# Optimization experiments

Hardware: AMD Instinct MI355X
Metric: run time of the kernel (lower is better)

The kernel has to match this reference:

```python
import jax, jax.numpy as jnp
import numpy as np

INT8_MAX = 127.0

def _quant_ste(x, axis):
    """Dynamic symmetric int8 fake-quant along `axis` (per-channel scales).
    Returns dequantized values; math matches int8 dot * scales (AQT-style)."""
    amax = jnp.max(jnp.abs(x), axis=axis, keepdims=True)
    scale = jnp.maximum(amax, 1e-6) / INT8_MAX
    q = jnp.clip(jnp.round(x / scale), -INT8_MAX, INT8_MAX)
    return q * scale

def setup_inputs() -> dict:
    key = jax.random.key(0)
    k1, k2 = jax.random.split(key)
    inputs = jax.random.normal(k1, (4, 2048, 4096), dtype=jnp.float32)
    kernel = jax.random.normal(k2, (4096, 4096), dtype=jnp.float32) * 0.02
    return {"inputs": inputs, "kernel": kernel}

def reference(inputs, kernel):
    # eqn: '...y,yz->...z' with quantized dot_general:
    # per-row (last-axis) dynamic int8 quant of activations,
    # per-output-column int8 quant of kernel, int8 matmul, dequant by scales.
    xq = _quant_ste(inputs, axis=-1)   # [B, S, D]
    kq = _quant_ste(kernel, axis=0)    # [D, F]
    return jnp.einsum('bsd,df->bsf', xq, kq)  # [B, S, F]
```

## Files before the change

### kernel.cpp

```cpp
#include <hip/hip_runtime.h>


#define M_DIM 8192
#define K_DIM 4096
#define N_DIM 4096

typedef int v4i __attribute__((ext_vector_type(4)));
typedef __attribute__((address_space(3))) void lds_void_t;
typedef const __attribute__((address_space(1))) void g_void_t;

__global__ void fused_qa(const float* __restrict__ X,
                         signed char* __restrict__ At,
                         float* __restrict__ sx,
                         const float* __restrict__ W,
                         float* __restrict__ part) {
  const int t = threadIdx.x;
  __shared__ float red[4];
  __shared__ float s_inv;
  __shared__ __align__(16) unsigned int shuf[1024];

  if (blockIdx.x < 128) {
    const int f4 = (blockIdx.x & 3) * 256 + t;
    const int slab = blockIdx.x >> 2;
    const float4* p = (const float4*)W + (size_t)slab * 128 * 1024 + f4;
    float4 a0 = {0.f, 0.f, 0.f, 0.f}, a1 = {0.f, 0.f, 0.f, 0.f};
#pragma unroll 8
    for (int i = 0; i < 64; ++i) {
      float4 u = p[(size_t)(2 * i) * 1024];
      float4 v = p[(size_t)(2 * i + 1) * 1024];
      a0.x = fmaxf(a0.x, fabsf(u.x));
      a0.y = fmaxf(a0.y, fabsf(u.y));
      a0.z = fmaxf(a0.z, fabsf(u.z));
      a0.w = fmaxf(a0.w, fabsf(u.w));
      a1.x = fmaxf(a1.x, fabsf(v.x));
      a1.y = fmaxf(a1.y, fabsf(v.y));
      a1.z = fmaxf(a1.z, fabsf(v.z));
      a1.w = fmaxf(a1.w, fabsf(v.w));
    }
    float4 r;
    r.x = fmaxf(a0.x, a1.x);
    r.y = fmaxf(a0.y, a1.y);
    r.z = fmaxf(a0.z, a1.z);
    r.w = fmaxf(a0.w, a1.w);
    ((float4*)part)[(size_t)slab * 1024 + f4] = r;
    return;
  }

  const int row = blockIdx.x - 128;
  const float* xr = X + (size_t)row * K_DIM;
  float4 v[4];
  float am = 0.f;
#pragma unroll
  for (int c = 0; c < 4; ++c) {
    v[c] = ((const float4*)xr)[c * 256 + t];
    am = fmaxf(am, fmaxf(fmaxf(fabsf(v[c].x), fabsf(v[c].y)),
                         fmaxf(fabsf(v[c].z), fabsf(v[c].w))));
  }
#pragma unroll
  for (int off = 32; off > 0; off >>= 1)
    am = fmaxf(am, __shfl_down(am, off));
  if ((t & 63) == 0) red[t >> 6] = am;
  __syncthreads();
  if (t == 0) {
    float m = fmaxf(fmaxf(red[0], red[1]), fmaxf(red[2], red[3]));
    float scale = fmaxf(m, 1e-6f) / 127.0f;
    sx[row] = scale;
    s_inv = 1.0f / scale;
  }
  __syncthreads();
  const float inv = s_inv;
#pragma unroll
  for (int c = 0; c < 4; ++c) {
    int q0 = (int)fminf(fmaxf(rintf(v[c].x * inv), -127.f), 127.f);
    int q1 = (int)fminf(fmaxf(rintf(v[c].y * inv), -127.f), 127.f);
    int q2 = (int)fminf(fmaxf(rintf(v[c].z * inv), -127.f), 127.f);
    int q3 = (int)fminf(fmaxf(rintf(v[c].w * inv), -127.f), 127.f);
    shuf[c * 256 + t] = (q0 & 255) | ((q1 & 255) << 8) | ((q2 & 255) << 16) | (q3 << 24);
  }
  __syncthreads();
  v4i w = *(const v4i*)&shuf[t * 4];
  signed char* dst = At + (size_t)(row >> 4) * 65536 + (t >> 2) * 1024 +
                     (row & 15) * 64 + (t & 3) * 16;
  *(v4i*)dst = w;
}

__global__ void wk_quant(const float* __restrict__ W,
                         const float* __restrict__ part,
                         signed char* __restrict__ Bt,
                         float* __restrict__ sk) {
  const int bx = blockIdx.x;
  const int f0 = (bx & 63) * 64;
  const int d0 = (bx >> 6) * 64;
  const int t = threadIdx.x;
  const int fl4 = t & 15;
  const int dl0 = t >> 4;
  __shared__ __align__(16) signed char tile[64 * 80];
  __shared__ float sl_inv[64];

  float4 wv[4];
#pragma unroll
  for (int c = 0; c < 4; ++c) {
    const int dl = c * 16 + dl0;
    wv[c] = ((const float4*)W)[(size_t)(d0 + dl) * 1024 + (f0 >> 2) + fl4];
  }
  if (t < 64) {
    const int f = f0 + t;
    float m = 0.f;
#pragma unroll
    for (int s = 0; s < 32; ++s) m = fmaxf(m, part[(size_t)s * 4096 + f]);
    const float scale = fmaxf(m, 1e-6f) / 127.0f;
    if (bx < 64) sk[f] = scale;
    sl_inv[t] = 1.0f / scale;
  }
  __syncthreads();
  const float4 inv4 = *(const float4*)&sl_inv[fl4 * 4];
#pragma unroll
  for (int c = 0; c < 4; ++c) {
    const int dl = c * 16 + dl0;
    tile[(fl4 * 4 + 0) * 80 + dl] =
        (signed char)(int)fminf(fmaxf(rintf(wv[c].x * inv4.x), -127.f), 127.f);
    tile[(fl4 * 4 + 1) * 80 + dl] =
        (signed char)(int)fminf(fmaxf(rintf(wv[c].y * inv4.y), -127.f), 127.f);
    tile[(fl4 * 4 + 2) * 80 + dl] =
        (signed char)(int)fminf(fmaxf(rintf(wv[c].z * inv4.z), -127.f), 127.f);
    tile[(fl4 * 4 + 3) * 80 + dl] =
        (signed char)(int)fminf(fmaxf(rintf(wv[c].w * inv4.w), -127.f), 127.f);
  }
  __syncthreads();
  const int frow = t >> 2;
  const int ksl = t & 3;
  v4i w = *(const v4i*)&tile[frow * 80 + ksl * 16];
  signed char* dst = Bt + (size_t)((f0 + frow) >> 4) * 65536 + (d0 >> 6) * 1024 +
                     (frow & 15) * 64 + ksl * 16;
  *(v4i*)dst = w;
}

__global__ __launch_bounds__(256, 2) void gemm_i8(
    const signed char* __restrict__ At, const signed char* __restrict__ Bt,
    const float* __restrict__ sx, const float* __restrict__ sk,
    float* __restrict__ C) {
  const int n0 = blockIdx.x * 128;
  const int m0 = blockIdx.y * 128;
  const int t = threadIdx.x;
  const int lane = t & 63;
  const int wave = t >> 6;
  const int wm = (wave >> 1) * 64;
  const int wn = (wave & 1) * 64;
  const int lrow = lane & 15;
  const int lq = lane >> 4;

  __shared__ __align__(16) signed char lds[32768];
  signed char* lA = lds;
  signed char* lB = lds + 16384;

  v4i acc[4][4];
#pragma unroll
  for (int i = 0; i < 4; ++i)
#pragma unroll
    for (int j = 0; j < 4; ++j) acc[i][j] = (v4i){0, 0, 0, 0};

  const signed char* Abase = At + (size_t)(m0 >> 4) * 65536;
  const signed char* Bbase = Bt + (size_t)(n0 >> 4) * 65536;

  const int la = ((wave >> 1) * 4) * 2048 + lane * 16;
  const int lb = ((wave & 1) * 4) * 2048 + lane * 16;

  for (int kb = 0; kb < K_DIM; kb += 128) {
    const int kofs = kb * 16;
#pragma unroll
    for (int j = 0; j < 4; ++j) {
      const int c = j * 256 + t;
      const int mt_i = c >> 7;
      const int off = ((c >> 6) & 1) * 1024 + (c & 15) * 64 + ((c >> 4) & 3) * 16;
      __builtin_amdgcn_global_load_lds(
          (g_void_t*)(Abase + (size_t)mt_i * 65536 + kofs + off),
          (lds_void_t*)(lA + c * 16), 16, 0, 0);
      __builtin_amdgcn_global_load_lds(
          (g_void_t*)(Bbase + (size_t)mt_i * 65536 + kofs + off),
          (lds_void_t*)(lB + c * 16), 16, 0, 0);
    }
    __syncthreads();
#pragma unroll
    for (int s = 0; s < 2; ++s) {
      v4i af[4], bf[4];
#pragma unroll
      for (int i = 0; i < 4; ++i) af[i] = *(const v4i*)(lA + la + i * 2048 + s * 1024);
#pragma unroll
      for (int i = 0; i < 4; ++i) bf[i] = *(const v4i*)(lB + lb + i * 2048 + s * 1024);
#pragma unroll
      for (int mi = 0; mi < 4; ++mi)
#pragma unroll
        for (int ni = 0; ni < 4; ++ni)
          acc[mi][ni] =
              __builtin_amdgcn_mfma_i32_16x16x64_i8(af[mi], bf[ni], acc[mi][ni], 0, 0, 0);
    }
    __syncthreads();
  }

#pragma unroll
  for (int mi = 0; mi < 4; ++mi) {
#pragma unroll
    for (int ni = 0; ni < 4; ++ni) {
      const int gn = n0 + wn + ni * 16 + lrow;
      const float skv = sk[gn];
#pragma unroll
      for (int r = 0; r < 4; ++r) {
        const int gm = m0 + wm + mi * 16 + lq * 4 + r;
        C[(size_t)gm * N_DIM + gn] = (float)acc[mi][ni][r] * sx[gm] * skv;
      }
    }
  }
}

extern "C" void kernel_launch(void* const* d_in, const int* in_sizes, int n_in,
                              void* d_out, int out_size, void* d_ws, size_t ws_size,
                              hipStream_t stream) {
  const float* X = (const float*)d_in[0];
  const float* W = (const float*)d_in[1];
  float* out = (float*)d_out;
  char* ws = (char*)d_ws;

  signed char* At = (signed char*)ws;
  signed char* Bt = (signed char*)(ws + 33554432);
  float* sx = (float*)(ws + 50331648);
  float* sk = (float*)(ws + 50364416);
  float* part = (float*)(ws + 50380800);

  fused_qa<<<8320, 256, 0, stream>>>(X, At, sx, W, part);
  wk_quant<<<4096, 256, 0, stream>>>(W, part, Bt, sk);
  gemm_i8<<<dim3(N_DIM / 128, M_DIM / 128), 256, 0, stream>>>(At, Bt, sx, sk, out);
}
```

Baseline: 432.0 us.

## Split activation quant into amax and quant passes with new int8 tile layout

The fused per-row activation kernel is replaced by two kernels. The first computes per-row amax and scale, with one half-wave per row. The second re-reads X and writes the int8 tiles directly in a new 16-byte-chunk layout, with no LDS shuffle. The B tile layout and the GEMM's global-to-LDS load addressing change to match, giving contiguous per-block 2KB loads. The cost is reading the 128MB activation tensor twice and one extra launch, in exchange for simpler stores and simpler GEMM load addressing.

```diff
diff --git a/kernel.cpp b/kernel.cpp
--- a/kernel.cpp
+++ b/kernel.cpp
@@ -9,15 +9,11 @@
 typedef __attribute__((address_space(3))) void lds_void_t;
 typedef const __attribute__((address_space(1))) void g_void_t;
 
-__global__ void fused_qa(const float* __restrict__ X,
-                         signed char* __restrict__ At,
-                         float* __restrict__ sx,
-                         const float* __restrict__ W,
-                         float* __restrict__ part) {
-  const int t = threadIdx.x;
-  __shared__ float red[4];
-  __shared__ float s_inv;
-  __shared__ __align__(16) unsigned int shuf[1024];
+__global__ void amax_pass(const float* __restrict__ X,
+                          float* __restrict__ sx, float* __restrict__ sxinv,
+                          const float* __restrict__ W,
+                          float* __restrict__ part) {
+  const int t = threadIdx.x;
 
   if (blockIdx.x < 128) {
     const int f4 = (blockIdx.x & 3) * 256 + t;
@@ -46,42 +42,52 @@
     return;
   }
 
-  const int row = blockIdx.x - 128;
-  const float* xr = X + (size_t)row * K_DIM;
-  float4 v[4];
+  const int row = (blockIdx.x - 128) * 8 + (t >> 5);
+  const int j = t & 31;
+  const float4* xr = (const float4*)X + (size_t)row * 1024;
   float am = 0.f;
-#pragma unroll
-  for (int c = 0; c < 4; ++c) {
-    v[c] = ((const float4*)xr)[c * 256 + t];
-    am = fmaxf(am, fmaxf(fmaxf(fabsf(v[c].x), fabsf(v[c].y)),
-                         fmaxf(fabsf(v[c].z), fabsf(v[c].w))));
-  }
-#pragma unroll
-  for (int off = 32; off > 0; off >>= 1)
-    am = fmaxf(am, __shfl_down(am, off));
-  if ((t & 63) == 0) red[t >> 6] = am;
-  __syncthreads();
-  if (t == 0) {
-    float m = fmaxf(fmaxf(red[0], red[1]), fmaxf(red[2], red[3]));
-    float scale = fmaxf(m, 1e-6f) / 127.0f;
+#pragma unroll 8
+  for (int i = 0; i < 32; ++i) {
+    float4 v = xr[j + 32 * i];
+    am = fmaxf(am, fmaxf(fmaxf(fabsf(v.x), fabsf(v.y)),
+                         fmaxf(fabsf(v.z), fabsf(v.w))));
+  }
+#pragma unroll
+  for (int off = 16; off > 0; off >>= 1)
+    am = fmaxf(am, __shfl_down(am, off, 32));
+  if (j == 0) {
+    float scale = fmaxf(am, 1e-6f) / 127.0f;
     sx[row] = scale;
-    s_inv = 1.0f / scale;
-  }
-  __syncthreads();
-  const float inv = s_inv;
-#pragma unroll
-  for (int c = 0; c < 4; ++c) {
-    int q0 = (int)fminf(fmaxf(rintf(v[c].x * inv), -127.f), 127.f);
-    int q1 = (int)fminf(fmaxf(rintf(v[c].y * inv), -127.f), 127.f);
-    int q2 = (int)fminf(fmaxf(rintf(v[c].z * inv), -127.f), 127.f);
-    int q3 = (int)fminf(fmaxf(rintf(v[c].w * inv), -127.f), 127.f);
-    shuf[c * 256 + t] = (q0 & 255) | ((q1 & 255) << 8) | ((q2 & 255) << 16) | (q3 << 24);
-  }
-  __syncthreads();
-  v4i w = *(const v4i*)&shuf[t * 4];
-  signed char* dst = At + (size_t)(row >> 4) * 65536 + (t >> 2) * 1024 +
-                     (row & 15) * 64 + (t & 3) * 16;
-  *(v4i*)dst = w;
+    sxinv[row] = 1.0f / scale;
+  }
+}
+
+__global__ void act_quant(const float* __restrict__ X,
+                          const float* __restrict__ sxinv,
+                          signed char* __restrict__ At) {
+  const int t = threadIdx.x;
+  const int row = t >> 4;
+  const int j = t & 15;
+  const int r0 = blockIdx.x * 16;
+  const float inv = sxinv[r0 + row];
+  const float4* xr = (const float4*)X + (size_t)(r0 + row) * 1024;
+  signed char* tile = At + (size_t)blockIdx.x * 65536 + row * 16;
+#pragma unroll 4
+  for (int u = 0; u < 16; ++u) {
+    const int s = u * 16 + j;
+    unsigned int d[4];
+#pragma unroll
+    for (int c = 0; c < 4; ++c) {
+      float4 v = xr[s * 4 + c];
+      int q0 = (int)fminf(fmaxf(rintf(v.x * inv), -127.f), 127.f);
+      int q1 = (int)fminf(fmaxf(rintf(v.y * inv), -127.f), 127.f);
+      int q2 = (int)fminf(fmaxf(rintf(v.z * inv), -127.f), 127.f);
+      int q3 = (int)fminf(fmaxf(rintf(v.w * inv), -127.f), 127.f);
+      d[c] = (q0 & 255) | ((q1 & 255) << 8) | ((q2 & 255) << 16) | (q3 << 24);
+    }
+    v4i w = {(int)d[0], (int)d[1], (int)d[2], (int)d[3]};
+    *(v4i*)(tile + s * 256) = w;
+  }
 }
 
 __global__ void wk_quant(const float* __restrict__ W,
@@ -130,8 +136,9 @@
   const int frow = t >> 2;
   const int ksl = t & 3;
   v4i w = *(const v4i*)&tile[frow * 80 + ksl * 16];
-  signed char* dst = Bt + (size_t)((f0 + frow) >> 4) * 65536 + (d0 >> 6) * 1024 +
-                     (frow & 15) * 64 + ksl * 16;
+  const int f = f0 + frow;
+  signed char* dst = Bt + (size_t)(f >> 4) * 65536 + ((d0 >> 4) + ksl) * 256 +
+                     (f & 15) * 16;
   *(v4i*)dst = w;
 }
 
@@ -171,12 +178,12 @@
     for (int j = 0; j < 4; ++j) {
       const int c = j * 256 + t;
       const int mt_i = c >> 7;
-      const int off = ((c >> 6) & 1) * 1024 + (c & 15) * 64 + ((c >> 4) & 3) * 16;
+      const int inner = c & 127;
       __builtin_amdgcn_global_load_lds(
-          (g_void_t*)(Abase + (size_t)mt_i * 65536 + kofs + off),
+          (g_void_t*)(Abase + (size_t)mt_i * 65536 + kofs + inner * 16),
           (lds_void_t*)(lA + c * 16), 16, 0, 0);
       __builtin_amdgcn_global_load_lds(
-          (g_void_t*)(Bbase + (size_t)mt_i * 65536 + kofs + off),
+          (g_void_t*)(Bbase + (size_t)mt_i * 65536 + kofs + inner * 16),
           (lds_void_t*)(lB + c * 16), 16, 0, 0);
     }
     __syncthreads();
@@ -223,10 +230,12 @@
   signed char* At = (signed char*)ws;
   signed char* Bt = (signed char*)(ws + 33554432);
   float* sx = (float*)(ws + 50331648);
-  float* sk = (float*)(ws + 50364416);
-  float* part = (float*)(ws + 50380800);
-
-  fused_qa<<<8320, 256, 0, stream>>>(X, At, sx, W, part);
+  float* sxinv = (float*)(ws + 50364416);
+  float* sk = (float*)(ws + 50397184);
+  float* part = (float*)(ws + 50413568);
+
+  amax_pass<<<1152, 256, 0, stream>>>(X, sx, sxinv, W, part);
+  act_quant<<<512, 256, 0, stream>>>(X, sxinv, At);
   wk_quant<<<4096, 256, 0, stream>>>(W, part, Bt, sk);
   gemm_i8<<<dim3(N_DIM / 128, M_DIM / 128), 256, 0, stream>>>(At, Bt, sx, sk, out);
 }
```

New measurement: 443.6 us. 2.7% more time.

## Repack int8 operand layout and process 16 rows per activation-quant block

Applied to the files above, without the earlier changes.

Changes the packed int8 tile layout for A and B so that each 16-byte chunk sits contiguously by k-slice. GEMM loads then become a linear 16-byte stride instead of a scattered offset formula. The activation quant kernel now handles 16 rows per 1024-thread block, one wave per row. This removes block-level reductions and the LDS shuffle, and each lane writes packed bytes straight to the new layout. Column-amax blocks shrink to 32 with 1024 threads each, which reduces parallelism for that part of the work.

```diff
diff --git a/kernel.cpp b/kernel.cpp
--- a/kernel.cpp
+++ b/kernel.cpp
@@ -9,79 +9,66 @@
 typedef __attribute__((address_space(3))) void lds_void_t;
 typedef const __attribute__((address_space(1))) void g_void_t;
 
-__global__ void fused_qa(const float* __restrict__ X,
-                         signed char* __restrict__ At,
-                         float* __restrict__ sx,
-                         const float* __restrict__ W,
-                         float* __restrict__ part) {
+__global__ __launch_bounds__(1024) void fused_prep(
+    const float* __restrict__ X, const float* __restrict__ W,
+    signed char* __restrict__ At, float* __restrict__ sx,
+    float* __restrict__ part) {
   const int t = threadIdx.x;
-  __shared__ float red[4];
-  __shared__ float s_inv;
-  __shared__ __align__(16) unsigned int shuf[1024];
-
-  if (blockIdx.x < 128) {
-    const int f4 = (blockIdx.x & 3) * 256 + t;
-    const int slab = blockIdx.x >> 2;
-    const float4* p = (const float4*)W + (size_t)slab * 128 * 1024 + f4;
-    float4 a0 = {0.f, 0.f, 0.f, 0.f}, a1 = {0.f, 0.f, 0.f, 0.f};
+
+  if (blockIdx.x < 32) {
+    const int slab = blockIdx.x;
+    const float4* p = (const float4*)W + (size_t)slab * 128 * 1024 + t;
+    float4 a = {0.f, 0.f, 0.f, 0.f};
 #pragma unroll 8
-    for (int i = 0; i < 64; ++i) {
-      float4 u = p[(size_t)(2 * i) * 1024];
-      float4 v = p[(size_t)(2 * i + 1) * 1024];
-      a0.x = fmaxf(a0.x, fabsf(u.x));
-      a0.y = fmaxf(a0.y, fabsf(u.y));
-      a0.z = fmaxf(a0.z, fabsf(u.z));
-      a0.w = fmaxf(a0.w, fabsf(u.w));
-      a1.x = fmaxf(a1.x, fabsf(v.x));
-      a1.y = fmaxf(a1.y, fabsf(v.y));
-      a1.z = fmaxf(a1.z, fabsf(v.z));
-      a1.w = fmaxf(a1.w, fabsf(v.w));
-    }
-    float4 r;
-    r.x = fmaxf(a0.x, a1.x);
-    r.y = fmaxf(a0.y, a1.y);
-    r.z = fmaxf(a0.z, a1.z);
-    r.w = fmaxf(a0.w, a1.w);
-    ((float4*)part)[(size_t)slab * 1024 + f4] = r;
+    for (int i = 0; i < 128; ++i) {
+      float4 u = p[(size_t)i * 1024];
+      a.x = fmaxf(a.x, fabsf(u.x));
+      a.y = fmaxf(a.y, fabsf(u.y));
+      a.z = fmaxf(a.z, fabsf(u.z));
+      a.w = fmaxf(a.w, fabsf(u.w));
+    }
+    ((float4*)part)[(size_t)slab * 1024 + t] = a;
     return;
   }
 
-  const int row = blockIdx.x - 128;
-  const float* xr = X + (size_t)row * K_DIM;
-  float4 v[4];
+  const int tile = blockIdx.x - 32;
+  const int row = t >> 6;
+  const int j = t & 63;
+  const float4* xr = (const float4*)X + ((size_t)tile * 16 + row) * 1024;
+
+  float4 v[4][4];
   float am = 0.f;
 #pragma unroll
-  for (int c = 0; c < 4; ++c) {
-    v[c] = ((const float4*)xr)[c * 256 + t];
-    am = fmaxf(am, fmaxf(fmaxf(fabsf(v[c].x), fabsf(v[c].y)),
-                         fmaxf(fabsf(v[c].z), fabsf(v[c].w))));
-  }
+  for (int u = 0; u < 4; ++u)
+#pragma unroll
+    for (int c = 0; c < 4; ++c) {
+      v[u][c] = xr[(u * 64 + j) * 4 + c];
+      am = fmaxf(am, fmaxf(fmaxf(fabsf(v[u][c].x), fabsf(v[u][c].y)),
+                           fmaxf(fabsf(v[u][c].z), fabsf(v[u][c].w))));
+    }
 #pragma unroll
   for (int off = 32; off > 0; off >>= 1)
     am = fmaxf(am, __shfl_down(am, off));
-  if ((t & 63) == 0) red[t >> 6] = am;
-  __syncthreads();
-  if (t == 0) {
-    float m = fmaxf(fmaxf(red[0], red[1]), fmaxf(red[2], red[3]));
-    float scale = fmaxf(m, 1e-6f) / 127.0f;
-    sx[row] = scale;
-    s_inv = 1.0f / scale;
-  }
-  __syncthreads();
-  const float inv = s_inv;
-#pragma unroll
-  for (int c = 0; c < 4; ++c) {
-    int q0 = (int)fminf(fmaxf(rintf(v[c].x * inv), -127.f), 127.f);
-    int q1 = (int)fminf(fmaxf(rintf(v[c].y * inv), -127.f), 127.f);
-    int q2 = (int)fminf(fmaxf(rintf(v[c].z * inv), -127.f), 127.f);
-    int q3 = (int)fminf(fmaxf(rintf(v[c].w * inv), -127.f), 127.f);
-    shuf[c * 256 + t] = (q0 & 255) | ((q1 & 255) << 8) | ((q2 & 255) << 16) | (q3 << 24);
-  }
-  __syncthreads();
-  v4i w = *(const v4i*)&shuf[t * 4];
-  signed char* dst = At + (size_t)(row >> 4) * 65536 + (t >> 2) * 1024 +
-                     (row & 15) * 64 + (t & 3) * 16;
-  *(v4i*)dst = w;
+  am = __shfl(am, 0);
+  const float scale = fmaxf(am, 1e-6f) / 127.0f;
+  if (j == 0) sx[tile * 16 + row] = scale;
+  const float inv = 1.0f / scale;
+
+  signed char* tb = At + (size_t)tile * 65536 + row * 16;
+#pragma unroll
+  for (int u = 0; u < 4; ++u) {
+    unsigned int d[4];
+#pragma unroll
+    for (int c = 0; c < 4; ++c) {
+      int q0 = (int)fminf(fmaxf(rintf(v[u][c].x * inv), -127.f), 127.f);
+      int q1 = (int)fminf(fmaxf(rintf(v[u][c].y * inv), -127.f), 127.f);
+      int q2 = (int)fminf(fmaxf(rintf(v[u][c].z * inv), -127.f), 127.f);
+      int q3 = (int)fminf(fmaxf(rintf(v[u][c].w * inv), -127.f), 127.f);
+      d[c] = (q0 & 255) | ((q1 & 255) << 8) | ((q2 & 255) << 16) | (q3 << 24);
+    }
+    v4i w = {(int)d[0], (int)d[1], (int)d[2], (int)d[3]};
+    *(v4i*)(tb + (u * 64 + j) * 256) = w;
+  }
 }
 
 __global__ void wk_quant(const float* __restrict__ W,
@@ -130,8 +117,9 @@
   const int frow = t >> 2;
   const int ksl = t & 3;
   v4i w = *(const v4i*)&tile[frow * 80 + ksl * 16];
-  signed char* dst = Bt + (size_t)((f0 + frow) >> 4) * 65536 + (d0 >> 6) * 1024 +
-                     (frow & 15) * 64 + ksl * 16;
+  const int f = f0 + frow;
+  signed char* dst = Bt + (size_t)(f >> 4) * 65536 + ((d0 >> 4) + ksl) * 256 +
+                     (f & 15) * 16;
   *(v4i*)dst = w;
 }
 
@@ -171,12 +159,12 @@
     for (int j = 0; j < 4; ++j) {
       const int c = j * 256 + t;
       const int mt_i = c >> 7;
-      const int off = ((c >> 6) & 1) * 1024 + (c & 15) * 64 + ((c >> 4) & 3) * 16;
+      const int inner = c & 127;
       __builtin_amdgcn_global_load_lds(
-          (g_void_t*)(Abase + (size_t)mt_i * 65536 + kofs + off),
+          (g_void_t*)(Abase + (size_t)mt_i * 65536 + kofs + inner * 16),
           (lds_void_t*)(lA + c * 16), 16, 0, 0);
       __builtin_amdgcn_global_load_lds(
-          (g_void_t*)(Bbase + (size_t)mt_i * 65536 + kofs + off),
+          (g_void_t*)(Bbase + (size_t)mt_i * 65536 + kofs + inner * 16),
           (lds_void_t*)(lB + c * 16), 16, 0, 0);
     }
     __syncthreads();
@@ -226,7 +214,7 @@
   float* sk = (float*)(ws + 50364416);
   float* part = (float*)(ws + 50380800);
 
-  fused_qa<<<8320, 256, 0, stream>>>(X, At, sx, W, part);
+  fused_prep<<<544, 1024, 0, stream>>>(X, W, At, sx, part);
   wk_quant<<<4096, 256, 0, stream>>>(W, part, Bt, sk);
   gemm_i8<<<dim3(N_DIM / 128, M_DIM / 128), 256, 0, stream>>>(At, Bt, sx, sk, out);
 }
```

Result: no change. 426.5 us (-1.3%).
